# Kernel tuning notes

Measured on AMD Instinct MI355X. Metric: run time of the kernel, lower is better.

The kernel has to match this reference:

```python
import jax, jax.numpy as jnp
import numpy as np
from jax import lax

EMBED = 768
D_INNER = 2 * EMBED          # expand = 2
D_STATE = 16
D_CONV = 4
DT_RANK = (EMBED + 15) // 16  # 48
FF = 3072
B, L = 2, 1024


def setup_inputs() -> dict:
    key = jax.random.key(0)
    ks = jax.random.split(key, 20)
    s = 0.02
    inp = {
        "x": jax.random.normal(ks[0], (B, L, EMBED), jnp.float32),
        # Mamba params
        "in_proj_w": jax.random.normal(ks[1], (2 * D_INNER, EMBED), jnp.float32) * s,
        "conv_w": jax.random.normal(ks[2], (D_INNER, 1, D_CONV), jnp.float32) * s,
        "conv_b": jnp.zeros((D_INNER,), jnp.float32),
        "x_proj_w": jax.random.normal(ks[3], (DT_RANK + 2 * D_STATE, D_INNER), jnp.float32) * s,
        "dt_proj_w": jax.random.normal(ks[4], (D_INNER, DT_RANK), jnp.float32) * s,
        "dt_proj_b": jax.random.normal(ks[5], (D_INNER,), jnp.float32) * s,
        "A_log": jnp.log(jnp.broadcast_to(jnp.arange(1, D_STATE + 1, dtype=jnp.float32), (D_INNER, D_STATE))),
        "D_param": jnp.ones((D_INNER,), jnp.float32),
        "out_proj_w": jax.random.normal(ks[6], (EMBED, D_INNER), jnp.float32) * s,
        # block params
        "ln1_w": jnp.ones((EMBED,), jnp.float32), "ln1_b": jnp.zeros((EMBED,), jnp.float32),
        "ln2_w": jnp.ones((EMBED,), jnp.float32), "ln2_b": jnp.zeros((EMBED,), jnp.float32),
        "ffn_w1": jax.random.normal(ks[7], (FF, EMBED), jnp.float32) * s,
        "ffn_b1": jnp.zeros((FF,), jnp.float32),
        "ffn_w2": jax.random.normal(ks[8], (EMBED, FF), jnp.float32) * s,
        "ffn_b2": jnp.zeros((EMBED,), jnp.float32),
    }
    return inp


def _layernorm(x, w, b, eps=1e-5):
    mu = jnp.mean(x, -1, keepdims=True)
    var = jnp.mean((x - mu) ** 2, -1, keepdims=True)
    return (x - mu) * lax.rsqrt(var + eps) * w + b


def _mamba(x, in_proj_w, conv_w, conv_b, x_proj_w, dt_proj_w, dt_proj_b,
           A_log, D_param, out_proj_w):
    # x: [B, L, E]
    xz = jnp.einsum('ble,de->bld', x, in_proj_w)          # [B,L,2*Di]
    xin, z = jnp.split(xz, 2, axis=-1)                    # [B,L,Di] each
    # causal depthwise conv over time
    xc = lax.conv_general_dilated(
        xin.transpose(0, 2, 1), conv_w, window_strides=(1,),
        padding=[(D_CONV - 1, 0)], feature_group_count=D_INNER,
        dimension_numbers=('NCH', 'OIH', 'NCH'))
    xc = (xc + conv_b[None, :, None]).transpose(0, 2, 1)  # [B,L,Di]
    xc = jax.nn.silu(xc)
    # input-dependent SSM params
    x_dbl = jnp.einsum('bld,rd->blr', xc, x_proj_w)       # [B,L,dt_rank+2n]
    dt, Bm, Cm = jnp.split(x_dbl, [DT_RANK, DT_RANK + D_STATE], axis=-1)
    delta = jax.nn.softplus(jnp.einsum('blr,dr->bld', dt, dt_proj_w) + dt_proj_b)
    A = -jnp.exp(A_log)                                   # [Di, n]
    deltaA = jnp.exp(jnp.einsum('bld,dn->bldn', delta, A))
    deltaBu = jnp.einsum('bld,bln,bld->bldn', delta, Bm, xc)

    def step(h, xs):
        dA, dBu, Ct = xs                                  # [B,Di,n],[B,Di,n],[B,n]
        h = dA * h + dBu
        y = jnp.einsum('bdn,bn->bd', h, Ct)
        return h, y

    h0 = jnp.zeros((x.shape[0], D_INNER, D_STATE), x.dtype)
    _, ys = lax.scan(step, h0, (deltaA.transpose(1, 0, 2, 3),
                                deltaBu.transpose(1, 0, 2, 3),
                                Cm.transpose(1, 0, 2)))
    y = ys.transpose(1, 0, 2)                             # [B,L,Di]
    y = y + xc * D_param
    y = y * jax.nn.silu(z)
    return jnp.einsum('bld,ed->ble', y, out_proj_w)


def reference(x, in_proj_w, conv_w, conv_b, x_proj_w, dt_proj_w, dt_proj_b,
              A_log, D_param, out_proj_w, ln1_w, ln1_b, ln2_w, ln2_b,
              ffn_w1, ffn_b1, ffn_w2, ffn_b2):
    # dropout is identity in eval mode
    h = _mamba(x, in_proj_w, conv_w, conv_b, x_proj_w, dt_proj_w, dt_proj_b,
               A_log, D_param, out_proj_w)
    x1 = _layernorm(h + x, ln1_w, ln1_b)
    f = jnp.einsum('ble,fe->blf', x1, ffn_w1) + ffn_b1
    f = jax.nn.gelu(f)
    f = jnp.einsum('blf,ef->ble', f, ffn_w2) + ffn_b2
    return _layernorm(f + x1, ln2_w, ln2_b)
```

## Files before the change

kernel.cpp:

```cpp
#include <hip/hip_runtime.h>
#include <math.h>

#define EMBED 768
#define DI 1536
#define DSTATE 16
#define DCONV 4
#define DTRANK 48
#define FF 3072
#define BATCH 2
#define SEQ 1024
#define NROWS (BATCH*SEQ)
#define TCH 32
#define NCH (SEQ/TCH)
#define DBLK 64

typedef __bf16 bf16x8 __attribute__((ext_vector_type(8)));
typedef float f32x4 __attribute__((ext_vector_type(4)));
typedef unsigned int u32x4 __attribute__((ext_vector_type(4)));

static __device__ __forceinline__ unsigned short f2b(float f) {
    union { float f; unsigned u; } v; v.f = f;
    unsigned r = v.u + 0x7FFFu + ((v.u >> 16) & 1u);
    return (unsigned short)(r >> 16);
}
static __device__ __forceinline__ float b2f(unsigned short s) {
    union { unsigned u; float f; } v; v.u = ((unsigned)s) << 16;
    return v.f;
}

#define GLOAD_LDS16(g, l) __builtin_amdgcn_global_load_lds( \
    (const __attribute__((address_space(1))) void*)(g), \
    (__attribute__((address_space(3))) void*)(l), 16, 0, 0)

template<int EPI, int KSPLIT>
__global__ __launch_bounds__(256)
void gemm_sk(const unsigned short* __restrict__ A,
             const unsigned short* __restrict__ W,
             float* __restrict__ C, unsigned short* __restrict__ Cb,
             float* __restrict__ part,
             int M, int N, int K,
             const float* __restrict__ bias)
{
    __shared__ alignas(16) unsigned short As[128 * 32];
    __shared__ alignas(16) unsigned short Ws[64 * 32];
    const int tid  = threadIdx.x;
    const int lane = tid & 63, wave = tid >> 6;
    const int bm = blockIdx.y * 128, bn = blockIdx.x * 64;
    const int kc = K / KSPLIT;
    const int kz = blockIdx.z * kc;
    const int ln = lane & 15, lg = lane >> 4;

    f32x4 acc[2][4];
    #pragma unroll
    for (int i = 0; i < 2; ++i)
        #pragma unroll
        for (int j = 0; j < 4; ++j)
            acc[i][j] = (f32x4){0.f, 0.f, 0.f, 0.f};

    const int ra = tid >> 2, ca = tid & 3;
    const int cs = (ca * 8) ^ ((ra & 3) << 3);
    const unsigned short* gA0 = A + (size_t)(bm + ra) * K + kz + cs;
    const unsigned short* gA1 = A + (size_t)(bm + ra + 64) * K + kz + cs;
    const unsigned short* gW  = W + (size_t)(bn + ra) * K + kz + cs;
    unsigned short* ldsA0 = As + wave * 512;
    unsigned short* ldsA1 = As + 2048 + wave * 512;
    unsigned short* ldsW  = Ws + wave * 512;

    for (int k0 = 0; k0 < kc; k0 += 32) {
        GLOAD_LDS16(gA0 + k0, ldsA0);
        GLOAD_LDS16(gA1 + k0, ldsA1);
        GLOAD_LDS16(gW  + k0, ldsW);
        __syncthreads();
        bf16x8 af[2], wf[4];
        #pragma unroll
        for (int i = 0; i < 2; ++i) {
            int row = wave * 32 + i * 16 + ln;
            af[i] = *reinterpret_cast<const bf16x8*>(
                &As[row * 32 + ((lg * 8) ^ ((row & 3) << 3))]);
        }
        #pragma unroll
        for (int j = 0; j < 4; ++j) {
            int row = j * 16 + ln;
            wf[j] = *reinterpret_cast<const bf16x8*>(
                &Ws[row * 32 + ((lg * 8) ^ ((row & 3) << 3))]);
        }
        #pragma unroll
        for (int i = 0; i < 2; ++i)
            #pragma unroll
            for (int j = 0; j < 4; ++j)
                acc[i][j] = __builtin_amdgcn_mfma_f32_16x16x32_bf16(af[i], wf[j], acc[i][j], 0, 0, 0);
        __syncthreads();
    }

    if constexpr (KSPLIT > 1) {
        float* pb = part + (size_t)blockIdx.z * M * N;
        #pragma unroll
        for (int i = 0; i < 2; ++i)
            #pragma unroll
            for (int j = 0; j < 4; ++j) {
                int col = bn + j * 16 + ln;
                #pragma unroll
                for (int rr = 0; rr < 4; ++rr) {
                    int row = bm + wave * 32 + i * 16 + lg * 4 + rr;
                    pb[(size_t)row * N + col] = acc[i][j][rr];
                }
            }
    } else {
        #pragma unroll
        for (int i = 0; i < 2; ++i)
            #pragma unroll
            for (int j = 0; j < 4; ++j) {
                int col = bn + j * 16 + ln;
                #pragma unroll
                for (int rr = 0; rr < 4; ++rr) {
                    int row = bm + wave * 32 + i * 16 + lg * 4 + rr;
                    float v = acc[i][j][rr];
                    size_t o = (size_t)row * N + col;
                    if (EPI == 1) {
                        v += bias[col];
                        C[o] = (v > 20.f) ? v : log1pf(expf(v));
                    } else if (EPI == 3) {
                        v += bias[col];
                        float t = 0.7978845608028654f * (v + 0.044715f * v * v * v);
                        Cb[o] = f2b(0.5f * v * (1.f + tanhf(t)));
                    } else if (EPI == 5) {
                        if (col < DI) C[(size_t)row * DI + col] = v;
                        else          Cb[(size_t)row * DI + col - DI] = f2b(v);
                    } else {
                        C[o] = v;
                    }
                }
            }
    }
}

template<int KS, int EPI>
__global__ __launch_bounds__(256)
void reduce_k(const float* __restrict__ part, float* __restrict__ C,
              const float* __restrict__ bias, const float* __restrict__ resid,
              int MN, int N)
{
    int i4 = (blockIdx.x * 256 + threadIdx.x) * 4;
    float4 s = *reinterpret_cast<const float4*>(part + i4);
    #pragma unroll
    for (int z = 1; z < KS; ++z) {
        float4 p = *reinterpret_cast<const float4*>(part + (size_t)z * MN + i4);
        s.x += p.x; s.y += p.y; s.z += p.z; s.w += p.w;
    }
    float4 r = *reinterpret_cast<const float4*>(resid + i4);
    if (EPI == 4) {
        int col = i4 % N;
        s.x += bias[col];     s.y += bias[col + 1];
        s.z += bias[col + 2]; s.w += bias[col + 3];
    }
    s.x += r.x; s.y += r.y; s.z += r.z; s.w += r.w;
    *reinterpret_cast<float4*>(C + i4) = s;
}

__global__ __launch_bounds__(256)
void xproj_mfma(const unsigned short* __restrict__ A,
                const unsigned short* __restrict__ W,
                float* __restrict__ part)
{
    const int mt = blockIdx.x, s = blockIdx.y;
    const int lane = threadIdx.x & 63, wave = threadIdx.x >> 6;
    const int ln = lane & 15, lg = lane >> 4;
    const int row0 = mt * 128 + wave * 32;
    const int kb = s * 192;
    f32x4 acc[2][5];
    #pragma unroll
    for (int i = 0; i < 2; ++i)
        #pragma unroll
        for (int j = 0; j < 5; ++j)
            acc[i][j] = (f32x4){0.f, 0.f, 0.f, 0.f};

    for (int kk = 0; kk < 192; kk += 32) {
        const int k = kb + kk + lg * 8;
        bf16x8 af[2], wf[5];
        af[0] = *reinterpret_cast<const bf16x8*>(A + (size_t)(row0 + ln) * DI + k);
        af[1] = *reinterpret_cast<const bf16x8*>(A + (size_t)(row0 + 16 + ln) * DI + k);
        #pragma unroll
        for (int j = 0; j < 5; ++j)
            wf[j] = *reinterpret_cast<const bf16x8*>(W + (size_t)(j * 16 + ln) * DI + k);
        #pragma unroll
        for (int i = 0; i < 2; ++i)
            #pragma unroll
            for (int j = 0; j < 5; ++j)
                acc[i][j] = __builtin_amdgcn_mfma_f32_16x16x32_bf16(af[i], wf[j], acc[i][j], 0, 0, 0);
    }
    float* pb = part + (size_t)s * NROWS * 80;
    #pragma unroll
    for (int i = 0; i < 2; ++i)
        #pragma unroll
        for (int j = 0; j < 5; ++j)
            #pragma unroll
            for (int rr = 0; rr < 4; ++rr) {
                int row = row0 + i * 16 + lg * 4 + rr;
                int col = j * 16 + ln;
                pb[(size_t)row * 80 + col] = acc[i][j][rr];
            }
}

__global__ __launch_bounds__(256)
void xproj_reduce(const float* __restrict__ part, float* __restrict__ xdbl,
                  unsigned short* __restrict__ xdblb)
{
    int idx = blockIdx.x * 256 + threadIdx.x;
    float sum = 0.f;
    #pragma unroll
    for (int s = 0; s < 8; ++s) sum += part[(size_t)s * NROWS * 80 + idx];
    xdbl[idx] = sum;
    int col = idx % 80, row = idx / 80;
    if (col < 48)      xdblb[row * 64 + col] = f2b(sum);
    else if (col < 64) xdblb[row * 64 + col] = 0;
}

__global__ __launch_bounds__(256)
void cvt6_k(const float* __restrict__ x,  const float* __restrict__ w1,
            const float* __restrict__ w2, const float* __restrict__ w3,
            const float* __restrict__ w4, const float* __restrict__ w5,
            unsigned short* __restrict__ xb,  unsigned short* __restrict__ w1b,
            unsigned short* __restrict__ w2b, unsigned short* __restrict__ w3b,
            unsigned short* __restrict__ w4b, unsigned short* __restrict__ w5b)
{
    size_t i4 = ((size_t)blockIdx.x * 256 + threadIdx.x) * 4;
    const float* src; unsigned short* dst; size_t off;
    if      (i4 < 1572864u) { src = x;  dst = xb;  off = i4; }
    else if (i4 < 3932160u) { src = w1; dst = w1b; off = i4 - 1572864u; }
    else if (i4 < 5111808u) { src = w2; dst = w2b; off = i4 - 3932160u; }
    else if (i4 < 7471104u) { src = w3; dst = w3b; off = i4 - 5111808u; }
    else if (i4 < 9830400u) { src = w4; dst = w4b; off = i4 - 7471104u; }
    else                    { src = w5; dst = w5b; off = i4 - 9830400u; }
    float4 v = *reinterpret_cast<const float4*>(src + off);
    ushort4 u;
    u.x = f2b(v.x); u.y = f2b(v.y); u.z = f2b(v.z); u.w = f2b(v.w);
    *reinterpret_cast<ushort4*>(dst + off) = u;
}

__global__ __launch_bounds__(256)
void cvt_dtw(const float* __restrict__ w, unsigned short* __restrict__ wb)
{
    int idx = blockIdx.x * 256 + threadIdx.x;
    int row = idx >> 6, col = idx & 63;
    wb[idx] = (col < 48) ? f2b(w[row * 48 + col]) : (unsigned short)0;
}

__global__ __launch_bounds__(256)
void conv_silu_k(const float* __restrict__ xin, const float* __restrict__ cw,
                 const float* __restrict__ cb, float* __restrict__ xc,
                 unsigned short* __restrict__ xcb)
{
    int q = blockIdx.x * 256 + threadIdx.x;
    int d4 = (q * 4) % DI;
    int bt = (q * 4) / DI;
    int t  = bt % SEQ, b = bt / SEQ;
    const float* base = xin + ((size_t)b * SEQ + t) * DI + d4;
    float4 s3 = *reinterpret_cast<const float4*>(base);
    float4 acc = *reinterpret_cast<const float4*>(cb + d4);
    float4 wv0 = *reinterpret_cast<const float4*>(cw + (d4 + 0) * 4);
    float4 wv1 = *reinterpret_cast<const float4*>(cw + (d4 + 1) * 4);
    float4 wv2 = *reinterpret_cast<const float4*>(cw + (d4 + 2) * 4);
    float4 wv3 = *reinterpret_cast<const float4*>(cw + (d4 + 3) * 4);
    acc.x += wv0.w * s3.x; acc.y += wv1.w * s3.y; acc.z += wv2.w * s3.z; acc.w += wv3.w * s3.w;
    if (t >= 1) {
        float4 s = *reinterpret_cast<const float4*>(base - DI);
        acc.x += wv0.z * s.x; acc.y += wv1.z * s.y; acc.z += wv2.z * s.z; acc.w += wv3.z * s.w;
    }
    if (t >= 2) {
        float4 s = *reinterpret_cast<const float4*>(base - 2 * DI);
        acc.x += wv0.y * s.x; acc.y += wv1.y * s.y; acc.z += wv2.y * s.z; acc.w += wv3.y * s.w;
    }
    if (t >= 3) {
        float4 s = *reinterpret_cast<const float4*>(base - 3 * DI);
        acc.x += wv0.x * s.x; acc.y += wv1.x * s.y; acc.z += wv2.x * s.z; acc.w += wv3.x * s.w;
    }
    float4 v;
    v.x = acc.x / (1.f + __expf(-acc.x));
    v.y = acc.y / (1.f + __expf(-acc.y));
    v.z = acc.z / (1.f + __expf(-acc.z));
    v.w = acc.w / (1.f + __expf(-acc.w));
    size_t o = (size_t)bt * DI + d4;
    *reinterpret_cast<float4*>(xc + o) = v;
    ushort4 u; u.x = f2b(v.x); u.y = f2b(v.y); u.z = f2b(v.z); u.w = f2b(v.w);
    *reinterpret_cast<ushort4*>(xcb + o) = u;
}

__global__ __launch_bounds__(256)
void scan2_a(const float* __restrict__ delta, const float* __restrict__ xc,
             const float* __restrict__ xdbl,  const float* __restrict__ A_log,
             float* __restrict__ hfin, float* __restrict__ aprod)
{
    const int d0 = blockIdx.x * DBLK, ch = blockIdx.y, b = blockIdx.z;
    const int t0 = ch * TCH;
    __shared__ float del_s[TCH][DBLK + 4];
    __shared__ float xc_s[TCH][DBLK + 4];
    __shared__ float b_s[TCH][20];
    const int tid = threadIdx.x;
    {
        const int c4 = tid & 15, tr = tid >> 4;
        #pragma unroll
        for (int p = 0; p < 2; ++p) {
            int t = p * 16 + tr;
            size_t rowo = (size_t)(b * SEQ + t0 + t);
            *reinterpret_cast<float4*>(&del_s[t][c4 * 4]) =
                *reinterpret_cast<const float4*>(&delta[rowo * DI + d0 + c4 * 4]);
            *reinterpret_cast<float4*>(&xc_s[t][c4 * 4]) =
                *reinterpret_cast<const float4*>(&xc[rowo * DI + d0 + c4 * 4]);
        }
        const int cbq = tid & 3, tb = tid >> 2;
        if (tb < TCH) {
            size_t rowo = (size_t)(b * SEQ + t0 + tb);
            *reinterpret_cast<float4*>(&b_s[tb][cbq * 4]) =
                *reinterpret_cast<const float4*>(&xdbl[rowo * 80 + DTRANK + cbq * 4]);
        }
    }
    __syncthreads();
    const int lane = tid & 63, wave = tid >> 6;
    const int wd = wave * 16 + (lane >> 2);
    const int d = d0 + wd;
    const int nq = (lane & 3) * 4;
    float4 Av = *reinterpret_cast<const float4*>(&A_log[d * DSTATE + nq]);
    const float A0 = -__expf(Av.x), A1 = -__expf(Av.y), A2 = -__expf(Av.z), A3 = -__expf(Av.w);
    float h0_ = 0.f, h1_ = 0.f, h2_ = 0.f, h3_ = 0.f;
    float p0 = 1.f, p1 = 1.f, p2 = 1.f, p3 = 1.f;
    #pragma unroll 4
    for (int t = 0; t < TCH; ++t) {
        float dl = del_s[t][wd];
        float u  = dl * xc_s[t][wd];
        float4 bq = *reinterpret_cast<const float4*>(&b_s[t][nq]);
        float e0 = __expf(dl * A0), e1 = __expf(dl * A1);
        float e2 = __expf(dl * A2), e3 = __expf(dl * A3);
        h0_ = e0 * h0_ + u * bq.x; p0 *= e0;
        h1_ = e1 * h1_ + u * bq.y; p1 *= e1;
        h2_ = e2 * h2_ + u * bq.z; p2 *= e2;
        h3_ = e3 * h3_ + u * bq.w; p3 *= e3;
    }
    size_t o = ((size_t)((b * NCH + ch) * DI) + d) * DSTATE + nq;
    *reinterpret_cast<float4*>(&hfin[o])  = (float4){h0_, h1_, h2_, h3_};
    *reinterpret_cast<float4*>(&aprod[o]) = (float4){p0, p1, p2, p3};
}

__global__ __launch_bounds__(256)
void scan2_b(const float* __restrict__ hfin, const float* __restrict__ aprod,
             float* __restrict__ h0)
{
    int idx = blockIdx.x * 256 + threadIdx.x;
    int nq = (idx & 3) * 4;
    int d  = (idx >> 2) % DI;
    int b  = (idx >> 2) / DI;
    float4 h = {0.f, 0.f, 0.f, 0.f};
    #pragma unroll
    for (int ch = 0; ch < NCH; ++ch) {
        size_t o = ((size_t)((b * NCH + ch) * DI) + d) * DSTATE + nq;
        *reinterpret_cast<float4*>(&h0[o]) = h;
        float4 a = *reinterpret_cast<const float4*>(&aprod[o]);
        float4 f = *reinterpret_cast<const float4*>(&hfin[o]);
        h.x = a.x * h.x + f.x; h.y = a.y * h.y + f.y;
        h.z = a.z * h.z + f.z; h.w = a.w * h.w + f.w;
    }
}

__global__ __launch_bounds__(256)
void scan2_c(const float* __restrict__ delta, const float* __restrict__ xc,
             const float* __restrict__ xdbl,  const float* __restrict__ A_log,
             const float* __restrict__ Dp,    const unsigned short* __restrict__ zb,
             const float* __restrict__ h0,
             unsigned short* __restrict__ yb)
{
    const int d0 = blockIdx.x * DBLK, ch = blockIdx.y, b = blockIdx.z;
    const int t0 = ch * TCH;
    __shared__ float del_s[TCH][DBLK + 4];
    __shared__ float xc_s[TCH][DBLK + 4];
    __shared__ float b_s[TCH][20];
    __shared__ float c_s[TCH][20];
    __shared__ unsigned short z_s[TCH][DBLK + 8];
    const int tid = threadIdx.x;
    {
        const int c4 = tid & 15, tr = tid >> 4;
        #pragma unroll
        for (int p = 0; p < 2; ++p) {
            int t = p * 16 + tr;
            size_t rowo = (size_t)(b * SEQ + t0 + t);
            *reinterpret_cast<float4*>(&del_s[t][c4 * 4]) =
                *reinterpret_cast<const float4*>(&delta[rowo * DI + d0 + c4 * 4]);
            *reinterpret_cast<float4*>(&xc_s[t][c4 * 4]) =
                *reinterpret_cast<const float4*>(&xc[rowo * DI + d0 + c4 * 4]);
        }
        const int cbq = tid & 3, tb = tid >> 2;
        if (tb < TCH) {
            size_t rowo = (size_t)(b * SEQ + t0 + tb);
            *reinterpret_cast<float4*>(&b_s[tb][cbq * 4]) =
                *reinterpret_cast<const float4*>(&xdbl[rowo * 80 + DTRANK + cbq * 4]);
        } else {
            size_t rowo = (size_t)(b * SEQ + t0 + tb - TCH);
            *reinterpret_cast<float4*>(&c_s[tb - TCH][cbq * 4]) =
                *reinterpret_cast<const float4*>(&xdbl[rowo * 80 + DTRANK + DSTATE + cbq * 4]);
        }
        const int cz = tid & 7, tz = tid >> 3;
        size_t rz = (size_t)(b * SEQ + t0 + tz);
        *reinterpret_cast<u32x4*>(&z_s[tz][cz * 8]) =
            *reinterpret_cast<const u32x4*>(&zb[rz * DI + d0 + cz * 8]);
    }
    __syncthreads();
    const int lane = tid & 63, wave = tid >> 6;
    const int wd = wave * 16 + (lane >> 2);
    const int d = d0 + wd;
    const int nq = (lane & 3) * 4;
    float4 Av = *reinterpret_cast<const float4*>(&A_log[d * DSTATE + nq]);
    const float A0 = -__expf(Av.x), A1 = -__expf(Av.y), A2 = -__expf(Av.z), A3 = -__expf(Av.w);
    const float Dd = Dp[d];
    float4 h = *reinterpret_cast<const float4*>(
        &h0[((size_t)((b * NCH + ch) * DI) + d) * DSTATE + nq]);
    unsigned short* yrow = yb + (size_t)(b * SEQ + t0) * DI + d;
    #pragma unroll 4
    for (int t = 0; t < TCH; ++t) {
        float dl = del_s[t][wd];
        float xv = xc_s[t][wd];
        float u  = dl * xv;
        float4 bq = *reinterpret_cast<const float4*>(&b_s[t][nq]);
        float4 cq = *reinterpret_cast<const float4*>(&c_s[t][nq]);
        float e0 = __expf(dl * A0), e1 = __expf(dl * A1);
        float e2 = __expf(dl * A2), e3 = __expf(dl * A3);
        h.x = e0 * h.x + u * bq.x;
        h.y = e1 * h.y + u * bq.y;
        h.z = e2 * h.z + u * bq.z;
        h.w = e3 * h.w + u * bq.w;
        float py = h.x * cq.x + h.y * cq.y + h.z * cq.z + h.w * cq.w;
        py += __shfl_xor(py, 1);
        py += __shfl_xor(py, 2);
        if ((lane & 3) == 0) {
            float yv = py + xv * Dd;
            float zv = b2f(z_s[t][wd]);
            yv *= zv / (1.f + __expf(-zv));
            yrow[(size_t)t * DI] = f2b(yv);
        }
    }
}

__global__ __launch_bounds__(256)
void layernorm_k(const float* __restrict__ in, const float* __restrict__ w,
                 const float* __restrict__ bb, float* __restrict__ out,
                 unsigned short* __restrict__ outb)
{
    const int row = blockIdx.x;
    const float* xr = in + (size_t)row * EMBED;
    const int i0 = threadIdx.x, i1 = i0 + 256, i2 = i0 + 512;
    float v0 = xr[i0], v1 = xr[i1], v2 = xr[i2];
    float s  = v0 + v1 + v2;
    float s2 = v0 * v0 + v1 * v1 + v2 * v2;
    #pragma unroll
    for (int m = 1; m < 64; m <<= 1) {
        s  += __shfl_xor(s,  m);
        s2 += __shfl_xor(s2, m);
    }
    __shared__ float sh1[4], sh2[4];
    int wv = threadIdx.x >> 6;
    if ((threadIdx.x & 63) == 0) { sh1[wv] = s; sh2[wv] = s2; }
    __syncthreads();
    float S1 = sh1[0] + sh1[1] + sh1[2] + sh1[3];
    float S2 = sh2[0] + sh2[1] + sh2[2] + sh2[3];
    float mu  = S1 * (1.f / EMBED);
    float var = S2 * (1.f / EMBED) - mu * mu;
    float rs  = rsqrtf(var + 1e-5f);
    float* orow = out + (size_t)row * EMBED;
    float o0 = (v0 - mu) * rs * w[i0] + bb[i0];
    float o1 = (v1 - mu) * rs * w[i1] + bb[i1];
    float o2 = (v2 - mu) * rs * w[i2] + bb[i2];
    orow[i0] = o0; orow[i1] = o1; orow[i2] = o2;
    if (outb) {
        unsigned short* obr = outb + (size_t)row * EMBED;
        obr[i0] = f2b(o0); obr[i1] = f2b(o1); obr[i2] = f2b(o2);
    }
}

extern "C" void kernel_launch(void* const* d_in, const int* in_sizes, int n_in,
                              void* d_out, int out_size, void* d_ws, size_t ws_size,
                              hipStream_t stream)
{
    const float* x         = (const float*)d_in[0];
    const float* in_proj_w = (const float*)d_in[1];
    const float* conv_w    = (const float*)d_in[2];
    const float* conv_b    = (const float*)d_in[3];
    const float* x_proj_w  = (const float*)d_in[4];
    const float* dt_proj_w = (const float*)d_in[5];
    const float* dt_proj_b = (const float*)d_in[6];
    const float* A_log     = (const float*)d_in[7];
    const float* D_param   = (const float*)d_in[8];
    const float* out_proj_w= (const float*)d_in[9];
    const float* ln1_w     = (const float*)d_in[10];
    const float* ln1_b     = (const float*)d_in[11];
    const float* ln2_w     = (const float*)d_in[12];
    const float* ln2_b     = (const float*)d_in[13];
    const float* ffn_w1    = (const float*)d_in[14];
    const float* ffn_b1    = (const float*)d_in[15];
    const float* ffn_w2    = (const float*)d_in[16];
    const float* ffn_b2    = (const float*)d_in[17];
    float* out = (float*)d_out;

    char* Wp = (char*)d_ws;
    float*          xin   = (float*)         (Wp + 0);
    unsigned short* zbuf  = (unsigned short*)(Wp + 12582912);
    float*          xc    = (float*)         (Wp + 18874368);
    float*          xdbl  = (float*)         (Wp + 31457280);
    float*          delta = (float*)         (Wp + 32112640);
    unsigned short* ybb   = (unsigned short*)(Wp + 44695552);
    float*          hres  = (float*)         (Wp + 50987008);
    unsigned short* xb    = (unsigned short*)(Wp + 58851328);
    unsigned short* wib   = (unsigned short*)(Wp + 61997056);
    unsigned short* wob   = (unsigned short*)(Wp + 66715648);
    unsigned short* wf1b  = (unsigned short*)(Wp + 69074944);
    unsigned short* wf2b  = (unsigned short*)(Wp + 73793536);
    unsigned short* fbf   = (unsigned short*)(Wp + 0);
    float*          ores  = (float*)         (Wp + 12582912);
    float*          x1    = (float*)         (Wp + 32112640);
    unsigned short* x1b   = (unsigned short*)(Wp + 58851328);
    float*          part  = (float*)         (Wp + 0);
    unsigned short* xdblb = (unsigned short*)(Wp + 5242880);
    unsigned short* xcb   = (unsigned short*)(Wp + 58851328);
    unsigned short* xpwb  = (unsigned short*)(Wp + 50987008);
    unsigned short* wdtb  = (unsigned short*)(Wp + 51232768);
    float*          hfin  = (float*)         (Wp + 0);
    float*          aprod = (float*)         (Wp + 6291456);
    float*          h0    = (float*)         (Wp + 50987008);
    float*          part_op = (float*)       (Wp + 0);
    float*          part_f2 = (float*)       (Wp + 38404096);

    dim3 blk(256);

    cvt6_k<<<9720, blk, 0, stream>>>(x, in_proj_w, out_proj_w, ffn_w1, ffn_w2, x_proj_w,
                                     xb, wib, wob, wf1b, wf2b, xpwb);
    cvt_dtw<<<384, blk, 0, stream>>>(dt_proj_w, wdtb);

    gemm_sk<5, 1><<<dim3(48, 16, 1), blk, 0, stream>>>(xb, wib, xin, zbuf, nullptr,
                                                       NROWS, 2 * DI, EMBED, nullptr);

    conv_silu_k<<<(BATCH * SEQ * DI) / 1024, blk, 0, stream>>>(xin, conv_w, conv_b, xc, xcb);

    xproj_mfma<<<dim3(16, 8), blk, 0, stream>>>(xcb, xpwb, part);
    xproj_reduce<<<640, blk, 0, stream>>>(part, xdbl, xdblb);

    gemm_sk<1, 1><<<dim3(24, 16, 1), blk, 0, stream>>>(xdblb, wdtb, delta, nullptr, nullptr,
                                                       NROWS, DI, 64, dt_proj_b);

    scan2_a<<<dim3(DI / DBLK, NCH, BATCH), blk, 0, stream>>>(delta, xc, xdbl, A_log, hfin, aprod);
    scan2_b<<<48, blk, 0, stream>>>(hfin, aprod, h0);
    scan2_c<<<dim3(DI / DBLK, NCH, BATCH), blk, 0, stream>>>(delta, xc, xdbl, A_log, D_param,
                                                             zbuf, h0, ybb);

    gemm_sk<0, 4><<<dim3(12, 16, 4), blk, 0, stream>>>(ybb, wob, nullptr, nullptr, part_op,
                                                       NROWS, EMBED, DI, nullptr);
    reduce_k<4, 2><<<1536, blk, 0, stream>>>(part_op, hres, nullptr, x,
                                             NROWS * EMBED, EMBED);

    layernorm_k<<<NROWS, blk, 0, stream>>>(hres, ln1_w, ln1_b, x1, x1b);

    gemm_sk<3, 1><<<dim3(48, 16, 1), blk, 0, stream>>>(x1b, wf1b, nullptr, fbf, nullptr,
                                                       NROWS, FF, EMBED, ffn_b1);

    gemm_sk<0, 4><<<dim3(12, 16, 4), blk, 0, stream>>>(fbf, wf2b, nullptr, nullptr, part_f2,
                                                       NROWS, EMBED, FF, nullptr);
    reduce_k<4, 4><<<1536, blk, 0, stream>>>(part_f2, ores, ffn_b2, x1,
                                             NROWS * EMBED, EMBED);

    layernorm_k<<<NROWS, blk, 0, stream>>>(ores, ln2_w, ln2_b, out, nullptr);
}
```

Baseline: 217.6 us.

## Enlarge GEMM tiles, fuse split-K reduce with layernorm, merge conversion and scan kernels

```diff
diff --git a/kernel.cpp b/kernel.cpp
--- a/kernel.cpp
+++ b/kernel.cpp
@@ -34,25 +34,26 @@
 
 template<int EPI, int KSPLIT>
 __global__ __launch_bounds__(256)
-void gemm_sk(const unsigned short* __restrict__ A,
-             const unsigned short* __restrict__ W,
-             float* __restrict__ C, unsigned short* __restrict__ Cb,
-             float* __restrict__ part,
-             int M, int N, int K,
-             const float* __restrict__ bias)
+void gemm_b(const unsigned short* __restrict__ A,
+            const unsigned short* __restrict__ W,
+            float* __restrict__ C, unsigned short* __restrict__ Cb,
+            float* __restrict__ part,
+            int M, int N, int K,
+            const float* __restrict__ bias)
 {
     __shared__ alignas(16) unsigned short As[128 * 32];
-    __shared__ alignas(16) unsigned short Ws[64 * 32];
+    __shared__ alignas(16) unsigned short Ws[128 * 32];
     const int tid  = threadIdx.x;
     const int lane = tid & 63, wave = tid >> 6;
-    const int bm = blockIdx.y * 128, bn = blockIdx.x * 64;
+    const int wr = (wave >> 1) * 64, wc = (wave & 1) * 64;
+    const int bm = blockIdx.y * 128, bn = blockIdx.x * 128;
     const int kc = K / KSPLIT;
     const int kz = blockIdx.z * kc;
     const int ln = lane & 15, lg = lane >> 4;
 
-    f32x4 acc[2][4];
+    f32x4 acc[4][4];
     #pragma unroll
-    for (int i = 0; i < 2; ++i)
+    for (int i = 0; i < 4; ++i)
         #pragma unroll
         for (int j = 0; j < 4; ++j)
             acc[i][j] = (f32x4){0.f, 0.f, 0.f, 0.f};
@@ -61,31 +62,34 @@
     const int cs = (ca * 8) ^ ((ra & 3) << 3);
     const unsigned short* gA0 = A + (size_t)(bm + ra) * K + kz + cs;
     const unsigned short* gA1 = A + (size_t)(bm + ra + 64) * K + kz + cs;
-    const unsigned short* gW  = W + (size_t)(bn + ra) * K + kz + cs;
+    const unsigned short* gW0 = W + (size_t)(bn + ra) * K + kz + cs;
+    const unsigned short* gW1 = W + (size_t)(bn + ra + 64) * K + kz + cs;
     unsigned short* ldsA0 = As + wave * 512;
     unsigned short* ldsA1 = As + 2048 + wave * 512;
-    unsigned short* ldsW  = Ws + wave * 512;
+    unsigned short* ldsW0 = Ws + wave * 512;
+    unsigned short* ldsW1 = Ws + 2048 + wave * 512;
 
     for (int k0 = 0; k0 < kc; k0 += 32) {
         GLOAD_LDS16(gA0 + k0, ldsA0);
         GLOAD_LDS16(gA1 + k0, ldsA1);
-        GLOAD_LDS16(gW  + k0, ldsW);
+        GLOAD_LDS16(gW0 + k0, ldsW0);
+        GLOAD_LDS16(gW1 + k0, ldsW1);
         __syncthreads();
-        bf16x8 af[2], wf[4];
-        #pragma unroll
-        for (int i = 0; i < 2; ++i) {
-            int row = wave * 32 + i * 16 + ln;
+        bf16x8 af[4], wf[4];
+        #pragma unroll
+        for (int i = 0; i < 4; ++i) {
+            int row = wr + i * 16 + ln;
             af[i] = *reinterpret_cast<const bf16x8*>(
                 &As[row * 32 + ((lg * 8) ^ ((row & 3) << 3))]);
         }
         #pragma unroll
         for (int j = 0; j < 4; ++j) {
-            int row = j * 16 + ln;
+            int row = wc + j * 16 + ln;
             wf[j] = *reinterpret_cast<const bf16x8*>(
                 &Ws[row * 32 + ((lg * 8) ^ ((row & 3) << 3))]);
         }
         #pragma unroll
-        for (int i = 0; i < 2; ++i)
+        for (int i = 0; i < 4; ++i)
             #pragma unroll
             for (int j = 0; j < 4; ++j)
                 acc[i][j] = __builtin_amdgcn_mfma_f32_16x16x32_bf16(af[i], wf[j], acc[i][j], 0, 0, 0);
@@ -95,25 +99,25 @@
     if constexpr (KSPLIT > 1) {
         float* pb = part + (size_t)blockIdx.z * M * N;
         #pragma unroll
-        for (int i = 0; i < 2; ++i)
+        for (int i = 0; i < 4; ++i)
             #pragma unroll
             for (int j = 0; j < 4; ++j) {
-                int col = bn + j * 16 + ln;
+                int col = bn + wc + j * 16 + ln;
                 #pragma unroll
                 for (int rr = 0; rr < 4; ++rr) {
-                    int row = bm + wave * 32 + i * 16 + lg * 4 + rr;
+                    int row = bm + wr + i * 16 + lg * 4 + rr;
                     pb[(size_t)row * N + col] = acc[i][j][rr];
                 }
             }
     } else {
         #pragma unroll
-        for (int i = 0; i < 2; ++i)
+        for (int i = 0; i < 4; ++i)
             #pragma unroll
             for (int j = 0; j < 4; ++j) {
-                int col = bn + j * 16 + ln;
+                int col = bn + wc + j * 16 + ln;
                 #pragma unroll
                 for (int rr = 0; rr < 4; ++rr) {
-                    int row = bm + wave * 32 + i * 16 + lg * 4 + rr;
+                    int row = bm + wr + i * 16 + lg * 4 + rr;
                     float v = acc[i][j][rr];
                     size_t o = (size_t)row * N + col;
                     if (EPI == 1) {
@@ -134,27 +138,48 @@
     }
 }
 
-template<int KS, int EPI>
-__global__ __launch_bounds__(256)
-void reduce_k(const float* __restrict__ part, float* __restrict__ C,
-              const float* __restrict__ bias, const float* __restrict__ resid,
-              int MN, int N)
-{
-    int i4 = (blockIdx.x * 256 + threadIdx.x) * 4;
-    float4 s = *reinterpret_cast<const float4*>(part + i4);
+template<int KS, int BIAS>
+__global__ __launch_bounds__(256)
+void reduce_ln(const float* __restrict__ part, const float* __restrict__ resid,
+               const float* __restrict__ bias,
+               const float* __restrict__ w, const float* __restrict__ bb,
+               float* __restrict__ out, unsigned short* __restrict__ outb)
+{
+    const int row = blockIdx.x;
+    const size_t ro = (size_t)row * EMBED;
+    const int i0 = threadIdx.x, i1 = i0 + 256, i2 = i0 + 512;
+    float v0 = 0.f, v1 = 0.f, v2 = 0.f;
     #pragma unroll
-    for (int z = 1; z < KS; ++z) {
-        float4 p = *reinterpret_cast<const float4*>(part + (size_t)z * MN + i4);
-        s.x += p.x; s.y += p.y; s.z += p.z; s.w += p.w;
-    }
-    float4 r = *reinterpret_cast<const float4*>(resid + i4);
-    if (EPI == 4) {
-        int col = i4 % N;
-        s.x += bias[col];     s.y += bias[col + 1];
-        s.z += bias[col + 2]; s.w += bias[col + 3];
-    }
-    s.x += r.x; s.y += r.y; s.z += r.z; s.w += r.w;
-    *reinterpret_cast<float4*>(C + i4) = s;
+    for (int z = 0; z < KS; ++z) {
+        const float* p = part + (size_t)z * NROWS * EMBED + ro;
+        v0 += p[i0]; v1 += p[i1]; v2 += p[i2];
+    }
+    if (BIAS) { v0 += bias[i0]; v1 += bias[i1]; v2 += bias[i2]; }
+    v0 += resid[ro + i0]; v1 += resid[ro + i1]; v2 += resid[ro + i2];
+
+    float s  = v0 + v1 + v2;
+    float s2 = v0 * v0 + v1 * v1 + v2 * v2;
+    #pragma unroll
+    for (int m = 1; m < 64; m <<= 1) {
+        s  += __shfl_xor(s,  m);
+        s2 += __shfl_xor(s2, m);
+    }
+    __shared__ float sh1[4], sh2[4];
+    int wv = threadIdx.x >> 6;
+    if ((threadIdx.x & 63) == 0) { sh1[wv] = s; sh2[wv] = s2; }
+    __syncthreads();
+    float S1 = sh1[0] + sh1[1] + sh1[2] + sh1[3];
+    float S2 = sh2[0] + sh2[1] + sh2[2] + sh2[3];
+    float mu  = S1 * (1.f / EMBED);
+    float var = S2 * (1.f / EMBED) - mu * mu;
+    float rs  = rsqrtf(var + 1e-5f);
+    float o0 = (v0 - mu) * rs * w[i0] + bb[i0];
+    float o1 = (v1 - mu) * rs * w[i1] + bb[i1];
+    float o2 = (v2 - mu) * rs * w[i2] + bb[i2];
+    out[ro + i0] = o0; out[ro + i1] = o1; out[ro + i2] = o2;
+    if (outb) {
+        outb[ro + i0] = f2b(o0); outb[ro + i1] = f2b(o1); outb[ro + i2] = f2b(o2);
+    }
 }
 
 __global__ __launch_bounds__(256)
@@ -216,14 +241,28 @@
 }
 
 __global__ __launch_bounds__(256)
-void cvt6_k(const float* __restrict__ x,  const float* __restrict__ w1,
+void cvt7_k(const float* __restrict__ x,  const float* __restrict__ w1,
             const float* __restrict__ w2, const float* __restrict__ w3,
             const float* __restrict__ w4, const float* __restrict__ w5,
+            const float* __restrict__ w6,
             unsigned short* __restrict__ xb,  unsigned short* __restrict__ w1b,
             unsigned short* __restrict__ w2b, unsigned short* __restrict__ w3b,
-            unsigned short* __restrict__ w4b, unsigned short* __restrict__ w5b)
+            unsigned short* __restrict__ w4b, unsigned short* __restrict__ w5b,
+            unsigned short* __restrict__ w6b)
 {
     size_t i4 = ((size_t)blockIdx.x * 256 + threadIdx.x) * 4;
+    if (i4 >= 9953280u) {
+        int off = (int)(i4 - 9953280u);
+        if (off >= 98304) return;
+        int row = off >> 6, colb = off & 63;
+        ushort4 u = {0, 0, 0, 0};
+        if (colb < 48) {
+            float4 v = *reinterpret_cast<const float4*>(w6 + row * 48 + colb);
+            u.x = f2b(v.x); u.y = f2b(v.y); u.z = f2b(v.z); u.w = f2b(v.w);
+        }
+        *reinterpret_cast<ushort4*>(w6b + off) = u;
+        return;
+    }
     const float* src; unsigned short* dst; size_t off;
     if      (i4 < 1572864u) { src = x;  dst = xb;  off = i4; }
     else if (i4 < 3932160u) { src = w1; dst = w1b; off = i4 - 1572864u; }
@@ -238,14 +277,6 @@
 }
 
 __global__ __launch_bounds__(256)
-void cvt_dtw(const float* __restrict__ w, unsigned short* __restrict__ wb)
-{
-    int idx = blockIdx.x * 256 + threadIdx.x;
-    int row = idx >> 6, col = idx & 63;
-    wb[idx] = (col < 48) ? f2b(w[row * 48 + col]) : (unsigned short)0;
-}
-
-__global__ __launch_bounds__(256)
 void conv_silu_k(const float* __restrict__ xin, const float* __restrict__ cw,
                  const float* __restrict__ cb, float* __restrict__ xc,
                  unsigned short* __restrict__ xcb)
@@ -253,8 +284,8 @@
     int q = blockIdx.x * 256 + threadIdx.x;
     int d4 = (q * 4) % DI;
     int bt = (q * 4) / DI;
-    int t  = bt % SEQ, b = bt / SEQ;
-    const float* base = xin + ((size_t)b * SEQ + t) * DI + d4;
+    int t  = bt % SEQ;
+    const float* base = xin + (size_t)bt * DI + d4;
     float4 s3 = *reinterpret_cast<const float4*>(base);
     float4 acc = *reinterpret_cast<const float4*>(cb + d4);
     float4 wv0 = *reinterpret_cast<const float4*>(cw + (d4 + 0) * 4);
@@ -341,30 +372,10 @@
 }
 
 __global__ __launch_bounds__(256)
-void scan2_b(const float* __restrict__ hfin, const float* __restrict__ aprod,
-             float* __restrict__ h0)
-{
-    int idx = blockIdx.x * 256 + threadIdx.x;
-    int nq = (idx & 3) * 4;
-    int d  = (idx >> 2) % DI;
-    int b  = (idx >> 2) / DI;
-    float4 h = {0.f, 0.f, 0.f, 0.f};
-    #pragma unroll
-    for (int ch = 0; ch < NCH; ++ch) {
-        size_t o = ((size_t)((b * NCH + ch) * DI) + d) * DSTATE + nq;
-        *reinterpret_cast<float4*>(&h0[o]) = h;
-        float4 a = *reinterpret_cast<const float4*>(&aprod[o]);
-        float4 f = *reinterpret_cast<const float4*>(&hfin[o]);
-        h.x = a.x * h.x + f.x; h.y = a.y * h.y + f.y;
-        h.z = a.z * h.z + f.z; h.w = a.w * h.w + f.w;
-    }
-}
-
-__global__ __launch_bounds__(256)
 void scan2_c(const float* __restrict__ delta, const float* __restrict__ xc,
              const float* __restrict__ xdbl,  const float* __restrict__ A_log,
              const float* __restrict__ Dp,    const unsigned short* __restrict__ zb,
-             const float* __restrict__ h0,
+             const float* __restrict__ hfin,  const float* __restrict__ aprod,
              unsigned short* __restrict__ yb)
 {
     const int d0 = blockIdx.x * DBLK, ch = blockIdx.y, b = blockIdx.z;
@@ -401,16 +412,24 @@
         *reinterpret_cast<u32x4*>(&z_s[tz][cz * 8]) =
             *reinterpret_cast<const u32x4*>(&zb[rz * DI + d0 + cz * 8]);
     }
-    __syncthreads();
     const int lane = tid & 63, wave = tid >> 6;
     const int wd = wave * 16 + (lane >> 2);
     const int d = d0 + wd;
     const int nq = (lane & 3) * 4;
+
+    float4 h = {0.f, 0.f, 0.f, 0.f};
+    for (int cc = 0; cc < ch; ++cc) {
+        size_t o = ((size_t)((b * NCH + cc) * DI) + d) * DSTATE + nq;
+        float4 a = *reinterpret_cast<const float4*>(&aprod[o]);
+        float4 f = *reinterpret_cast<const float4*>(&hfin[o]);
+        h.x = a.x * h.x + f.x; h.y = a.y * h.y + f.y;
+        h.z = a.z * h.z + f.z; h.w = a.w * h.w + f.w;
+    }
+
     float4 Av = *reinterpret_cast<const float4*>(&A_log[d * DSTATE + nq]);
     const float A0 = -__expf(Av.x), A1 = -__expf(Av.y), A2 = -__expf(Av.z), A3 = -__expf(Av.w);
     const float Dd = Dp[d];
-    float4 h = *reinterpret_cast<const float4*>(
-        &h0[((size_t)((b * NCH + ch) * DI) + d) * DSTATE + nq]);
+    __syncthreads();
     unsigned short* yrow = yb + (size_t)(b * SEQ + t0) * DI + d;
     #pragma unroll 4
     for (int t = 0; t < TCH; ++t) {
@@ -437,42 +456,6 @@
     }
 }
 
-__global__ __launch_bounds__(256)
-void layernorm_k(const float* __restrict__ in, const float* __restrict__ w,
-                 const float* __restrict__ bb, float* __restrict__ out,
-                 unsigned short* __restrict__ outb)
-{
-    const int row = blockIdx.x;
-    const float* xr = in + (size_t)row * EMBED;
-    const int i0 = threadIdx.x, i1 = i0 + 256, i2 = i0 + 512;
-    float v0 = xr[i0], v1 = xr[i1], v2 = xr[i2];
-    float s  = v0 + v1 + v2;
-    float s2 = v0 * v0 + v1 * v1 + v2 * v2;
-    #pragma unroll
-    for (int m = 1; m < 64; m <<= 1) {
-        s  += __shfl_xor(s,  m);
-        s2 += __shfl_xor(s2, m);
-    }
-    __shared__ float sh1[4], sh2[4];
-    int wv = threadIdx.x >> 6;
-    if ((threadIdx.x & 63) == 0) { sh1[wv] = s; sh2[wv] = s2; }
-    __syncthreads();
-    float S1 = sh1[0] + sh1[1] + sh1[2] + sh1[3];
-    float S2 = sh2[0] + sh2[1] + sh2[2] + sh2[3];
-    float mu  = S1 * (1.f / EMBED);
-    float var = S2 * (1.f / EMBED) - mu * mu;
-    float rs  = rsqrtf(var + 1e-5f);
-    float* orow = out + (size_t)row * EMBED;
-    float o0 = (v0 - mu) * rs * w[i0] + bb[i0];
-    float o1 = (v1 - mu) * rs * w[i1] + bb[i1];
-    float o2 = (v2 - mu) * rs * w[i2] + bb[i2];
-    orow[i0] = o0; orow[i1] = o1; orow[i2] = o2;
-    if (outb) {
-        unsigned short* obr = outb + (size_t)row * EMBED;
-        obr[i0] = f2b(o0); obr[i1] = f2b(o1); obr[i2] = f2b(o2);
-    }
-}
-
 extern "C" void kernel_launch(void* const* d_in, const int* in_sizes, int n_in,
                               void* d_out, int out_size, void* d_ws, size_t ws_size,
                               hipStream_t stream)
@@ -504,14 +487,12 @@
     float*          xdbl  = (float*)         (Wp + 31457280);
     float*          delta = (float*)         (Wp + 32112640);
     unsigned short* ybb   = (unsigned short*)(Wp + 44695552);
-    float*          hres  = (float*)         (Wp + 50987008);
     unsigned short* xb    = (unsigned short*)(Wp + 58851328);
     unsigned short* wib   = (unsigned short*)(Wp + 61997056);
     unsigned short* wob   = (unsigned short*)(Wp + 66715648);
     unsigned short* wf1b  = (unsigned short*)(Wp + 69074944);
     unsigned short* wf2b  = (unsigned short*)(Wp + 73793536);
     unsigned short* fbf   = (unsigned short*)(Wp + 0);
-    float*          ores  = (float*)         (Wp + 12582912);
     float*          x1    = (float*)         (Wp + 32112640);
     unsigned short* x1b   = (unsigned short*)(Wp + 58851328);
     float*          part  = (float*)         (Wp + 0);
@@ -521,46 +502,37 @@
     unsigned short* wdtb  = (unsigned short*)(Wp + 51232768);
     float*          hfin  = (float*)         (Wp + 0);
     float*          aprod = (float*)         (Wp + 6291456);
-    float*          h0    = (float*)         (Wp + 50987008);
     float*          part_op = (float*)       (Wp + 0);
     float*          part_f2 = (float*)       (Wp + 38404096);
 
     dim3 blk(256);
 
-    cvt6_k<<<9720, blk, 0, stream>>>(x, in_proj_w, out_proj_w, ffn_w1, ffn_w2, x_proj_w,
-                                     xb, wib, wob, wf1b, wf2b, xpwb);
-    cvt_dtw<<<384, blk, 0, stream>>>(dt_proj_w, wdtb);
-
-    gemm_sk<5, 1><<<dim3(48, 16, 1), blk, 0, stream>>>(xb, wib, xin, zbuf, nullptr,
-                                                       NROWS, 2 * DI, EMBED, nullptr);
+    cvt7_k<<<9816, blk, 0, stream>>>(x, in_proj_w, out_proj_w, ffn_w1, ffn_w2, x_proj_w,
+                                     dt_proj_w, xb, wib, wob, wf1b, wf2b, xpwb, wdtb);
+
+    gemm_b<5, 1><<<dim3(24, 16, 1), blk, 0, stream>>>(xb, wib, xin, zbuf, nullptr,
+                                                      NROWS, 2 * DI, EMBED, nullptr);
 
     conv_silu_k<<<(BATCH * SEQ * DI) / 1024, blk, 0, stream>>>(xin, conv_w, conv_b, xc, xcb);
 
     xproj_mfma<<<dim3(16, 8), blk, 0, stream>>>(xcb, xpwb, part);
     xproj_reduce<<<640, blk, 0, stream>>>(part, xdbl, xdblb);
 
-    gemm_sk<1, 1><<<dim3(24, 16, 1), blk, 0, stream>>>(xdblb, wdtb, delta, nullptr, nullptr,
-                                                       NROWS, DI, 64, dt_proj_b);
+    gemm_b<1, 1><<<dim3(12, 16, 1), blk, 0, stream>>>(xdblb, wdtb, delta, nullptr, nullptr,
+                                                      NROWS, DI, 64, dt_proj_b);
 
     scan2_a<<<dim3(DI / DBLK, NCH, BATCH), blk, 0, stream>>>(delta, xc, xdbl, A_log, hfin, aprod);
-    scan2_b<<<48, blk, 0, stream>>>(hfin, aprod, h0);
     scan2_c<<<dim3(DI / DBLK, NCH, BATCH), blk, 0, stream>>>(delta, xc, xdbl, A_log, D_param,
-                                                             zbuf, h0, ybb);
-
-    gemm_sk<0, 4><<<dim3(12, 16, 4), blk, 0, stream>>>(ybb, wob, nullptr, nullptr, part_op,
-                                                       NROWS, EMBED, DI, nullptr);
-    reduce_k<4, 2><<<1536, blk, 0, stream>>>(part_op, hres, nullptr, x,
-                                             NROWS * EMBED, EMBED);
-
-    layernorm_k<<<NROWS, blk, 0, stream>>>(hres, ln1_w, ln1_b, x1, x1b);
-
-    gemm_sk<3, 1><<<dim3(48, 16, 1), blk, 0, stream>>>(x1b, wf1b, nullptr, fbf, nullptr,
-                                                       NROWS, FF, EMBED, ffn_b1);
-
-    gemm_sk<0, 4><<<dim3(12, 16, 4), blk, 0, stream>>>(fbf, wf2b, nullptr, nullptr, part_f2,
-                                                       NROWS, EMBED, FF, nullptr);
-    reduce_k<4, 4><<<1536, blk, 0, stream>>>(part_f2, ores, ffn_b2, x1,
-                                             NROWS * EMBED, EMBED);
-
-    layernorm_k<<<NROWS, blk, 0, stream>>>(ores, ln2_w, ln2_b, out, nullptr);
-}
+                                                             zbuf, hfin, aprod, ybb);
+
+    gemm_b<0, 4><<<dim3(6, 16, 4), blk, 0, stream>>>(ybb, wob, nullptr, nullptr, part_op,
+                                                     NROWS, EMBED, DI, nullptr);
+    reduce_ln<4, 0><<<NROWS, blk, 0, stream>>>(part_op, x, nullptr, ln1_w, ln1_b, x1, x1b);
+
+    gemm_b<3, 1><<<dim3(24, 16, 1), blk, 0, stream>>>(x1b, wf1b, nullptr, fbf, nullptr,
+                                                      NROWS, FF, EMBED, ffn_b1);
+
+    gemm_b<0, 4><<<dim3(6, 16, 4), blk, 0, stream>>>(fbf, wf2b, nullptr, nullptr, part_f2,
+                                                     NROWS, EMBED, FF, nullptr);
+    reduce_ln<4, 1><<<NROWS, blk, 0, stream>>>(part_f2, x1, ffn_b2, ln2_w, ln2_b, out, nullptr);
+}
```

New measurement: 229.9 us. 5.6% more time.
